# Optimization experiments

Measured on AMD Instinct MI355X. Metric: run time of the kernel, lower is better.

## Reference

```python
import math
import jax, jax.numpy as jnp
import numpy as np

B, T, D = 128, 243, 1024   # batch, motion frames, latent_dim
N, L = 77, 512             # text tokens, text_latent_dim
H = 16                     # num_head -> head_dim 64
EPS = 1e-5


def _ln(x, g, b):
    m = x.mean(-1, keepdims=True)
    v = jnp.var(x, axis=-1, keepdims=True)
    return (x - m) * jax.lax.rsqrt(v + EPS) * g + b


def setup_inputs() -> dict:
    key = jax.random.key(0)
    ks = jax.random.split(key, 16)
    s = 0.02
    return {
        "x": jax.random.normal(ks[0], (B, T, D), jnp.float32),
        "xf": jax.random.normal(ks[1], (B, N, L), jnp.float32),
        "emb": jax.random.normal(ks[2], (B, T, D), jnp.float32),
        "ln_g": jnp.ones((D,), jnp.float32), "ln_b": jnp.zeros((D,), jnp.float32),
        "tln_g": jnp.ones((L,), jnp.float32), "tln_b": jnp.zeros((L,), jnp.float32),
        "Wq": jax.random.normal(ks[3], (D, D), jnp.float32) * s,
        "bq": jnp.zeros((D,), jnp.float32),
        "Wk": jax.random.normal(ks[4], (L, D), jnp.float32) * s,
        "bk": jnp.zeros((D,), jnp.float32),
        "Wv": jax.random.normal(ks[5], (L, D), jnp.float32) * s,
        "bv": jnp.zeros((D,), jnp.float32),
        "We": jax.random.normal(ks[6], (D, 2 * D), jnp.float32) * s,  # emb_layers Linear(time_embed_dim=D, 2D)
        "be": jnp.zeros((2 * D,), jnp.float32),
        "ln2_g": jnp.ones((D,), jnp.float32), "ln2_b": jnp.zeros((D,), jnp.float32),
        "Wo": jax.random.normal(ks[7], (D, D), jnp.float32) * s,     # zero_module in torch; random here for non-trivial baseline
        "bo": jnp.zeros((D,), jnp.float32),
    }


def reference(x, xf, emb, ln_g, ln_b, tln_g, tln_b, Wq, bq, Wk, bk, Wv, bv,
              We, be, ln2_g, ln2_b, Wo, bo):
    B_, T_, D_ = x.shape
    dh = D_ // H
    # cross-attention: queries from motion tokens, keys/values from text
    q = (_ln(x, ln_g, ln_b) @ Wq + bq).reshape(B_, T_, H, dh)
    xfn = _ln(xf, tln_g, tln_b)
    k = (xfn @ Wk + bk).reshape(B_, -1, H, dh)
    v = (xfn @ Wv + bv).reshape(B_, -1, H, dh)
    att = jnp.einsum('bthd,bnhd->btnh', q, k) / math.sqrt(dh)  # (B,T,N,H)
    w = jax.nn.softmax(att, axis=2)                            # softmax over text tokens; dropout is eval-mode identity
    y = jnp.einsum('btnh,bnhd->bthd', w, v).reshape(B_, T_, D_)
    # StylizationBlock (AdaLN): emb viewed (B,T,D), only first timestep used
    emb_out = (jax.nn.silu(emb) @ We + be)[:, 0:1, :]          # (B,1,2D)
    scale, shift = jnp.split(emb_out, 2, axis=2)
    h = _ln(y, ln2_g, ln2_b) * (1.0 + scale) + shift
    h = jax.nn.silu(h) @ Wo + bo
    return x + h
```

## Files before the change

kernel.cpp:

```cpp
#include <hip/hip_runtime.h>
#include <cstdint>

typedef __attribute__((ext_vector_type(8))) __bf16 bf16x8;
typedef __attribute__((ext_vector_type(4))) float f32x4;
typedef __attribute__((ext_vector_type(8))) unsigned short ushort8v;

__device__ __forceinline__ float b2f(unsigned short u) {
    union { uint32_t i; float f; } w; w.i = ((uint32_t)u) << 16; return w.f;
}
__device__ __forceinline__ unsigned short f2b(float f) {
    union { uint32_t i; float f; } w; w.f = f;
    uint32_t r = (w.i + 0x7FFFu + ((w.i >> 16) & 1u)) >> 16;
    return (unsigned short)r;
}

__device__ __forceinline__ void gl16(const unsigned short* g, unsigned short* l) {
    __builtin_amdgcn_global_load_lds(
        (const __attribute__((address_space(1))) void*)g,
        (__attribute__((address_space(3))) void*)l,
        16, 0, 0);
}

__global__ __launch_bounds__(256) void k_cvt_all(
    const float* __restrict__ Wq, const float* __restrict__ Wk,
    const float* __restrict__ Wv, const float* __restrict__ We,
    const float* __restrict__ Wo,
    unsigned short* __restrict__ wqt, unsigned short* __restrict__ wkvt,
    unsigned short* __restrict__ wet, unsigned short* __restrict__ wot) {
    __shared__ float s[32][33];
    int bid = blockIdx.x;
    const float* in; unsigned short* out; int R, C;
    if (bid < 1024)      { in = Wq; out = wqt;              R = 1024; C = 1024; }
    else if (bid < 1536) { bid -= 1024; in = Wk; out = wkvt;             R = 512;  C = 1024; }
    else if (bid < 2048) { bid -= 1536; in = Wv; out = wkvt + 1024 * 512; R = 512;  C = 1024; }
    else if (bid < 4096) { bid -= 2048; in = We; out = wet;              R = 1024; C = 2048; }
    else                 { bid -= 4096; in = Wo; out = wot;              R = 1024; C = 1024; }
    const int ctiles = C >> 5;
    const int c0 = (bid % ctiles) * 32, r0 = (bid / ctiles) * 32;
    const int tx = threadIdx.x & 31, ty = threadIdx.x >> 5;
#pragma unroll
    for (int i = 0; i < 4; ++i)
        s[ty + i * 8][tx] = in[(size_t)(r0 + ty + i * 8) * C + c0 + tx];
    __syncthreads();
#pragma unroll
    for (int i = 0; i < 4; ++i)
        out[(size_t)(c0 + ty + i * 8) * R + r0 + tx] = f2b(s[tx][ty + i * 8]);
}

template <int DIM>
__global__ __launch_bounds__(256) void k_ln(const float* __restrict__ in,
                                            const float* __restrict__ g,
                                            const float* __restrict__ b,
                                            unsigned short* __restrict__ out) {
    const int row = blockIdx.x * 4 + (threadIdx.x >> 6);
    const int ln = threadIdx.x & 63;
    constexpr int PL = DIM / 64;
    float v[PL];
    const size_t base = (size_t)row * DIM + (size_t)ln * PL;
    const float4* p4 = (const float4*)(in + base);
#pragma unroll
    for (int c = 0; c < PL / 4; ++c) {
        const float4 t = p4[c];
        v[c * 4 + 0] = t.x; v[c * 4 + 1] = t.y; v[c * 4 + 2] = t.z; v[c * 4 + 3] = t.w;
    }
    float s = 0.f, s2 = 0.f;
#pragma unroll
    for (int c = 0; c < PL; ++c) { s += v[c]; s2 += v[c] * v[c]; }
    for (int o = 1; o < 64; o <<= 1) { s += __shfl_xor(s, o); s2 += __shfl_xor(s2, o); }
    const float mean = s / DIM;
    const float rstd = rsqrtf(s2 / DIM - mean * mean + 1e-5f);
    const float4* g4 = (const float4*)(g + ln * PL);
    const float4* b4 = (const float4*)(b + ln * PL);
#pragma unroll
    for (int c0 = 0; c0 < PL; c0 += 8) {
        ushort8v yv;
#pragma unroll
        for (int j = 0; j < 8; ++j) {
            const int c = c0 + j;
            const float gg = ((const float*)g4)[c];
            const float bb = ((const float*)b4)[c];
            yv[j] = f2b((v[c] - mean) * rstd * gg + bb);
        }
        *(ushort8v*)(out + base + c0) = yv;
    }
}

__global__ __launch_bounds__(256) void k_silu(const float* __restrict__ emb,
                                              unsigned short* __restrict__ se) {
    const int i = blockIdx.x * 256 + threadIdx.x;
    const int b = i >> 10, k = i & 1023;
    const float f = emb[(size_t)b * (243 * 1024) + k];
    se[i] = f2b(f / (1.f + __expf(-f)));
}

template <int EPI>
__global__ __launch_bounds__(512, 2) void k_mm(
    const unsigned short* __restrict__ A, const unsigned short* __restrict__ Bt,
    const float* __restrict__ bias0, const float* __restrict__ bias1,
    unsigned short* __restrict__ C0, unsigned short* __restrict__ C1,
    float* __restrict__ Cf, const float* __restrict__ X,
    int N, int K) {
    __shared__ __align__(16) unsigned short sA[128 * 64];
    __shared__ __align__(16) unsigned short sB[256 * 64];
    const int tid = threadIdx.x, wv = tid >> 6, ln = tid & 63;
    const int wm = wv >> 2, wn = wv & 3;
    const int ln15 = ln & 15, lg = ln >> 4;

    const int NN = N >> 8;
    const int nwg = gridDim.x;
    const int wg = blockIdx.x;
    const int q = nwg >> 3, r = nwg & 7;
    const int xcd = wg & 7, idx = wg >> 3;
    const int u = (xcd < r) ? (xcd * (q + 1) + idx)
                            : (r * (q + 1) + (xcd - r) * q + idx);
    const int m0 = (u / NN) * 128, n0 = (u % NN) * 256;

    const f32x4 fz = {0.f, 0.f, 0.f, 0.f};
    f32x4 acc[4][4];
#pragma unroll
    for (int i = 0; i < 4; ++i)
#pragma unroll
        for (int j = 0; j < 4; ++j) acc[i][j] = fz;

    const int lrow = ln >> 3;
    const int sslot = (ln & 7) ^ lrow;
    const unsigned short* ga = A + (size_t)(m0 + wv * 16 + lrow) * K + sslot * 8;
    const unsigned short* gb = Bt + (size_t)(n0 + wv * 32 + lrow) * K + sslot * 8;
    unsigned short* const lA = sA + (wv * 16) * 64;
    unsigned short* const lB = sB + (wv * 32) * 64;

    for (int k0 = 0; k0 < K; k0 += 64) {
#pragma unroll
        for (int i = 0; i < 2; ++i)
            gl16(ga + k0 + (size_t)i * 8 * K, lA + i * 8 * 64);
#pragma unroll
        for (int i = 0; i < 4; ++i)
            gl16(gb + k0 + (size_t)i * 8 * K, lB + i * 8 * 64);
        __syncthreads();
        bf16x8 af[4][2], bf[4][2];
#pragma unroll
        for (int i = 0; i < 4; ++i) {
            const int ra2 = wm * 64 + i * 16 + ln15;
            const int rb2 = wn * 64 + i * 16 + ln15;
#pragma unroll
            for (int ks = 0; ks < 2; ++ks) {
                const int slot = ks * 4 + lg;
                af[i][ks] = *(const bf16x8*)(sA + ra2 * 64 + ((slot ^ (ra2 & 7)) * 8));
                bf[i][ks] = *(const bf16x8*)(sB + rb2 * 64 + ((slot ^ (rb2 & 7)) * 8));
            }
        }
#pragma unroll
        for (int mi = 0; mi < 4; ++mi)
#pragma unroll
            for (int ni = 0; ni < 4; ++ni) {
                acc[mi][ni] = __builtin_amdgcn_mfma_f32_16x16x32_bf16(af[mi][0], bf[ni][0], acc[mi][ni], 0, 0, 0);
                acc[mi][ni] = __builtin_amdgcn_mfma_f32_16x16x32_bf16(af[mi][1], bf[ni][1], acc[mi][ni], 0, 0, 0);
            }
        __syncthreads();
    }

    const int colB = n0 + wn * 64;
    const int rowB = m0 + wm * 64;
#pragma unroll
    for (int mi = 0; mi < 4; ++mi) {
#pragma unroll
        for (int ni = 0; ni < 4; ++ni) {
            const int col = colB + ni * 16 + ln15;
            const int row = rowB + mi * 16 + lg * 4;
            float bvv;
            if (EPI == 2) bvv = (col < 1024) ? bias0[col] : bias1[col - 1024];
            else bvv = bias0[col];
#pragma unroll
            for (int r2 = 0; r2 < 4; ++r2) {
                const float v = acc[mi][ni][r2] + bvv;
                if (EPI == 0) {
                    C0[(size_t)(row + r2) * N + col] = f2b(v);
                } else if (EPI == 1) {
                    Cf[(size_t)(row + r2) * N + col] = v + X[(size_t)(row + r2) * N + col];
                } else if (EPI == 2) {
                    if (col < 1024) C0[(size_t)(row + r2) * 1024 + col] = f2b(v);
                    else C1[(size_t)(row + r2) * 1024 + (col - 1024)] = f2b(v);
                } else {
                    Cf[(size_t)(row + r2) * N + col] = v;
                }
            }
        }
    }
}

__global__ __launch_bounds__(256, 2) void k_attn_m(const unsigned short* __restrict__ Q,
                                                   const unsigned short* __restrict__ Kb,
                                                   const unsigned short* __restrict__ Vb,
                                                   unsigned short* __restrict__ Y) {
    __shared__ __align__(16) unsigned short sK[80 * 64];
    __shared__ __align__(16) unsigned short sV[64 * 96];
    __shared__ __align__(16) unsigned short sP[4][16 * 104];
    const int bh = blockIdx.x;
    const int b = bh >> 4, h = bh & 15;
    const int tid = threadIdx.x, wv = tid >> 6, ln = tid & 63;
    const int ln15 = ln & 15, lg = ln >> 4;

    for (int c = tid; c < 640; c += 256) {
        const int n = c >> 3, ci = c & 7;
        uint4 val = make_uint4(0u, 0u, 0u, 0u);
        if (n < 77) val = *(const uint4*)(Kb + (size_t)(b * 77 + n) * 1024 + h * 64 + ci * 8);
        *(uint4*)((char*)sK + n * 128 + ((ci * 16) ^ ((n & 7) << 4))) = val;
    }
    for (int i = tid; i < 64 * 96; i += 256) {
        const int d = i / 96, n = i - d * 96;
        unsigned short val = 0;
        if (n < 77) val = Vb[(size_t)(b * 77 + n) * 1024 + h * 64 + d];
        sV[i] = val;
    }
    for (int i = ln; i < 16 * 24; i += 64) {
        const int rr = i / 24, cc = i - rr * 24;
        sP[wv][rr * 104 + 80 + cc] = 0;
    }
    bf16x8 qf[4][2];
    const size_t qbase = (size_t)b * (243 * 1024) + h * 64;
#pragma unroll
    for (int mi = 0; mi < 4; ++mi) {
        int t = wv * 64 + mi * 16 + ln15;
        if (t > 242) t = 242;
#pragma unroll
        for (int ks = 0; ks < 2; ++ks)
            qf[mi][ks] = *(const bf16x8*)(Q + qbase + (size_t)t * 1024 + ks * 32 + lg * 8);
    }
    __syncthreads();

    const f32x4 fz = {0.f, 0.f, 0.f, 0.f};
    f32x4 yacc[4][4];
#pragma unroll
    for (int i = 0; i < 4; ++i)
#pragma unroll
        for (int j = 0; j < 4; ++j) yacc[i][j] = fz;

#pragma unroll
    for (int mi = 0; mi < 4; ++mi) {
        f32x4 sc[5];
#pragma unroll
        for (int ci = 0; ci < 5; ++ci) sc[ci] = fz;
#pragma unroll
        for (int ci = 0; ci < 5; ++ci) {
            const int n = ci * 16 + ln15;
#pragma unroll
            for (int ks = 0; ks < 2; ++ks) {
                const int kk = ks * 32 + lg * 8;
                bf16x8 kf = *(const bf16x8*)((const char*)sK + n * 128 + ((kk * 2) ^ ((n & 7) << 4)));
                sc[ci] = __builtin_amdgcn_mfma_f32_16x16x32_bf16(qf[mi][ks], kf, sc[ci], 0, 0, 0);
            }
        }
#pragma unroll
        for (int r = 0; r < 4; ++r) {
            float e[5];
            float mx = -1e30f;
#pragma unroll
            for (int ci = 0; ci < 5; ++ci) {
                const int n = ci * 16 + ln15;
                const float vv = (n < 77) ? sc[ci][r] * 0.125f : -1e30f;
                e[ci] = vv;
                mx = fmaxf(mx, vv);
            }
            mx = fmaxf(mx, __shfl_xor(mx, 1));
            mx = fmaxf(mx, __shfl_xor(mx, 2));
            mx = fmaxf(mx, __shfl_xor(mx, 4));
            mx = fmaxf(mx, __shfl_xor(mx, 8));
            float ssum = 0.f;
#pragma unroll
            for (int ci = 0; ci < 5; ++ci) {
                const int n = ci * 16 + ln15;
                const float ev = (n < 77) ? __expf(e[ci] - mx) : 0.f;
                e[ci] = ev;
                ssum += ev;
            }
            ssum += __shfl_xor(ssum, 1);
            ssum += __shfl_xor(ssum, 2);
            ssum += __shfl_xor(ssum, 4);
            ssum += __shfl_xor(ssum, 8);
            const float inv = 1.f / ssum;
            const int prow = lg * 4 + r;
#pragma unroll
            for (int ci = 0; ci < 5; ++ci)
                sP[wv][prow * 104 + ci * 16 + ln15] = f2b(e[ci] * inv);
        }
#pragma unroll
        for (int ks = 0; ks < 3; ++ks) {
            bf16x8 pa = *(const bf16x8*)(sP[wv] + ln15 * 104 + ks * 32 + lg * 8);
#pragma unroll
            for (int di = 0; di < 4; ++di) {
                bf16x8 vf = *(const bf16x8*)(sV + (di * 16 + ln15) * 96 + ks * 32 + lg * 8);
                yacc[mi][di] = __builtin_amdgcn_mfma_f32_16x16x32_bf16(pa, vf, yacc[mi][di], 0, 0, 0);
            }
        }
    }
    const size_t ybase = (size_t)b * (243 * 1024) + h * 64;
#pragma unroll
    for (int mi = 0; mi < 4; ++mi)
#pragma unroll
        for (int di = 0; di < 4; ++di)
#pragma unroll
            for (int r = 0; r < 4; ++r) {
                const int t = wv * 64 + mi * 16 + lg * 4 + r;
                if (t < 243) Y[ybase + (size_t)t * 1024 + di * 16 + ln15] = f2b(yacc[mi][di][r]);
            }
}

__global__ __launch_bounds__(256) void k_act(const unsigned short* __restrict__ y,
                                             const float* __restrict__ eo,
                                             const float* __restrict__ g,
                                             const float* __restrict__ b,
                                             unsigned short* __restrict__ out) {
    const int row = blockIdx.x * 4 + (threadIdx.x >> 6);
    const int ln = threadIdx.x & 63;
    const int bb = row / 243;
    float v[16];
    const size_t base = (size_t)row * 1024 + ln * 16;
#pragma unroll
    for (int c0 = 0; c0 < 16; c0 += 8) {
        const ushort8v t = *(const ushort8v*)(y + base + c0);
#pragma unroll
        for (int j = 0; j < 8; ++j) v[c0 + j] = b2f(t[j]);
    }
    float s = 0.f, s2 = 0.f;
#pragma unroll
    for (int c = 0; c < 16; ++c) { s += v[c]; s2 += v[c] * v[c]; }
    for (int o = 1; o < 64; o <<= 1) { s += __shfl_xor(s, o); s2 += __shfl_xor(s2, o); }
    const float mean = s / 1024.f;
    const float rstd = rsqrtf(s2 / 1024.f - mean * mean + 1e-5f);
    const float* gp = g + ln * 16;
    const float* bp = b + ln * 16;
    const float* sc = eo + (size_t)bb * 2048 + ln * 16;
    const float* sh = sc + 1024;
#pragma unroll
    for (int c0 = 0; c0 < 16; c0 += 8) {
        ushort8v yv;
#pragma unroll
        for (int j = 0; j < 8; ++j) {
            const int c = c0 + j;
            const float nl = (v[c] - mean) * rstd * gp[c] + bp[c];
            const float hh = nl * (1.f + sc[c]) + sh[c];
            yv[j] = f2b(hh / (1.f + __expf(-hh)));
        }
        *(ushort8v*)(out + base + c0) = yv;
    }
}

extern "C" void kernel_launch(void* const* d_in, const int* in_sizes, int n_in,
                              void* d_out, int out_size, void* d_ws, size_t ws_size,
                              hipStream_t stream) {
    (void)in_sizes; (void)n_in; (void)out_size; (void)ws_size;

    const float* x     = (const float*)d_in[0];
    const float* xf    = (const float*)d_in[1];
    const float* emb   = (const float*)d_in[2];
    const float* ln_g  = (const float*)d_in[3];
    const float* ln_b  = (const float*)d_in[4];
    const float* tln_g = (const float*)d_in[5];
    const float* tln_b = (const float*)d_in[6];
    const float* Wq    = (const float*)d_in[7];
    const float* bq    = (const float*)d_in[8];
    const float* Wk    = (const float*)d_in[9];
    const float* bk    = (const float*)d_in[10];
    const float* Wv    = (const float*)d_in[11];
    const float* bv    = (const float*)d_in[12];
    const float* We    = (const float*)d_in[13];
    const float* be    = (const float*)d_in[14];
    const float* ln2_g = (const float*)d_in[15];
    const float* ln2_b = (const float*)d_in[16];
    const float* Wo    = (const float*)d_in[17];
    const float* bo    = (const float*)d_in[18];
    float* outp = (float*)d_out;

    char* ws = (char*)d_ws;
    constexpr size_t o_wq   = 0;
    constexpr size_t o_wkv  = o_wq + 2097152;
    constexpr size_t o_we   = o_wkv + 2097152;
    constexpr size_t o_wo   = o_we + 4194304;
    constexpr size_t o_se   = o_wo + 2097152;
    constexpr size_t o_eo   = o_se + 262144;
    constexpr size_t o_xn   = o_eo + 1048576;
    constexpr size_t o_qb   = o_xn + 63700992;
    constexpr size_t o_xfn  = o_qb + 63700992;
    constexpr size_t o_kb   = o_xfn + 10092544;
    constexpr size_t o_vb   = o_kb + 20185088;

    unsigned short* wqt  = (unsigned short*)(ws + o_wq);
    unsigned short* wkvt = (unsigned short*)(ws + o_wkv);
    unsigned short* wet  = (unsigned short*)(ws + o_we);
    unsigned short* wot  = (unsigned short*)(ws + o_wo);
    unsigned short* se   = (unsigned short*)(ws + o_se);
    float*          eo   = (float*)(ws + o_eo);
    unsigned short* xn   = (unsigned short*)(ws + o_xn);
    unsigned short* yb   = xn;
    unsigned short* qb   = (unsigned short*)(ws + o_qb);
    unsigned short* actb = qb;
    unsigned short* xfn  = (unsigned short*)(ws + o_xfn);
    unsigned short* kb   = (unsigned short*)(ws + o_kb);
    unsigned short* vb   = (unsigned short*)(ws + o_vb);

    k_ln<1024><<<7776, 256, 0, stream>>>(x, ln_g, ln_b, xn);
    k_ln<512><<<2464, 256, 0, stream>>>(xf, tln_g, tln_b, xfn);
    k_silu<<<512, 256, 0, stream>>>(emb, se);
    k_cvt_all<<<5120, 256, 0, stream>>>(Wq, Wk, Wv, We, Wo, wqt, wkvt, wet, wot);

    k_mm<3><<<8, 512, 0, stream>>>(se, wet, be, nullptr,
                                   nullptr, nullptr, eo, nullptr, 2048, 1024);

    k_mm<0><<<243 * 4, 512, 0, stream>>>(xn, wqt, bq, nullptr,
                                         qb, nullptr, nullptr, nullptr, 1024, 1024);
    k_mm<2><<<77 * 8, 512, 0, stream>>>(xfn, wkvt, bk, bv,
                                        kb, vb, nullptr, nullptr, 2048, 512);

    k_attn_m<<<2048, 256, 0, stream>>>(qb, kb, vb, yb);

    k_act<<<7776, 256, 0, stream>>>(yb, eo, ln2_g, ln2_b, actb);

    k_mm<1><<<243 * 4, 512, 0, stream>>>(actb, wot, bo, nullptr,
                                         nullptr, nullptr, outp, x, 1024, 1024);
}
```

Before: 393.7 us.

## Merge Q, KV and emb GEMMs into one launch and coalesce attention I/O

After: 353.5 us. 1.11x faster.

```diff
diff --git a/kernel.cpp b/kernel.cpp
--- a/kernel.cpp
+++ b/kernel.cpp
@@ -19,6 +19,13 @@
         (const __attribute__((address_space(1))) void*)g,
         (__attribute__((address_space(3))) void*)l,
         16, 0, 0);
+}
+
+__device__ __forceinline__ int swz8(int wg, int nwg) {
+    const int q = nwg >> 3, r = nwg & 7;
+    const int xcd = wg & 7, idx = wg >> 3;
+    return (xcd < r) ? (xcd * (q + 1) + idx)
+                     : (r * (q + 1) + (xcd - r) * q + idx);
 }
 
 __global__ __launch_bounds__(256) void k_cvt_all(
@@ -93,26 +100,17 @@
     se[i] = f2b(f / (1.f + __expf(-f)));
 }
 
-template <int EPI>
-__global__ __launch_bounds__(512, 2) void k_mm(
+__device__ __forceinline__ void mm_body(
+    int u, int NN,
     const unsigned short* __restrict__ A, const unsigned short* __restrict__ Bt,
     const float* __restrict__ bias0, const float* __restrict__ bias1,
     unsigned short* __restrict__ C0, unsigned short* __restrict__ C1,
     float* __restrict__ Cf, const float* __restrict__ X,
-    int N, int K) {
-    __shared__ __align__(16) unsigned short sA[128 * 64];
-    __shared__ __align__(16) unsigned short sB[256 * 64];
+    int N, int K, int epi,
+    unsigned short* sA, unsigned short* sB) {
     const int tid = threadIdx.x, wv = tid >> 6, ln = tid & 63;
     const int wm = wv >> 2, wn = wv & 3;
     const int ln15 = ln & 15, lg = ln >> 4;
-
-    const int NN = N >> 8;
-    const int nwg = gridDim.x;
-    const int wg = blockIdx.x;
-    const int q = nwg >> 3, r = nwg & 7;
-    const int xcd = wg & 7, idx = wg >> 3;
-    const int u = (xcd < r) ? (xcd * (q + 1) + idx)
-                            : (r * (q + 1) + (xcd - r) * q + idx);
     const int m0 = (u / NN) * 128, n0 = (u % NN) * 256;
 
     const f32x4 fz = {0.f, 0.f, 0.f, 0.f};
@@ -168,16 +166,16 @@
             const int col = colB + ni * 16 + ln15;
             const int row = rowB + mi * 16 + lg * 4;
             float bvv;
-            if (EPI == 2) bvv = (col < 1024) ? bias0[col] : bias1[col - 1024];
+            if (epi == 2) bvv = (col < 1024) ? bias0[col] : bias1[col - 1024];
             else bvv = bias0[col];
 #pragma unroll
             for (int r2 = 0; r2 < 4; ++r2) {
                 const float v = acc[mi][ni][r2] + bvv;
-                if (EPI == 0) {
+                if (epi == 0) {
                     C0[(size_t)(row + r2) * N + col] = f2b(v);
-                } else if (EPI == 1) {
+                } else if (epi == 1) {
                     Cf[(size_t)(row + r2) * N + col] = v + X[(size_t)(row + r2) * N + col];
-                } else if (EPI == 2) {
+                } else if (epi == 2) {
                     if (col < 1024) C0[(size_t)(row + r2) * 1024 + col] = f2b(v);
                     else C1[(size_t)(row + r2) * 1024 + (col - 1024)] = f2b(v);
                 } else {
@@ -188,11 +186,45 @@
     }
 }
 
+__global__ __launch_bounds__(512, 2) void k_mm3(
+    const unsigned short* __restrict__ xn, const unsigned short* __restrict__ wqt,
+    const float* __restrict__ bq, unsigned short* __restrict__ qb,
+    const unsigned short* __restrict__ xfn, const unsigned short* __restrict__ wkvt,
+    const float* __restrict__ bk, const float* __restrict__ bv,
+    unsigned short* __restrict__ kb, unsigned short* __restrict__ vb,
+    const unsigned short* __restrict__ se, const unsigned short* __restrict__ wet,
+    const float* __restrict__ be, float* __restrict__ eo) {
+    __shared__ __align__(16) unsigned short sA[128 * 64];
+    __shared__ __align__(16) unsigned short sB[256 * 64];
+    const int wg = blockIdx.x;
+    if (wg < 972) {
+        mm_body(swz8(wg, 972), 4, xn, wqt, bq, nullptr, qb, nullptr, nullptr, nullptr,
+                1024, 1024, 0, sA, sB);
+    } else if (wg < 1588) {
+        mm_body(swz8(wg - 972, 616), 8, xfn, wkvt, bk, bv, kb, vb, nullptr, nullptr,
+                2048, 512, 2, sA, sB);
+    } else {
+        mm_body(wg - 1588, 8, se, wet, be, nullptr, nullptr, nullptr, eo, nullptr,
+                2048, 1024, 3, sA, sB);
+    }
+}
+
+__global__ __launch_bounds__(512, 2) void k_mm1(
+    const unsigned short* __restrict__ actb, const unsigned short* __restrict__ wot,
+    const float* __restrict__ bo, const float* __restrict__ x,
+    float* __restrict__ outp) {
+    __shared__ __align__(16) unsigned short sA[128 * 64];
+    __shared__ __align__(16) unsigned short sB[256 * 64];
+    mm_body(swz8(blockIdx.x, 972), 4, actb, wot, bo, nullptr, nullptr, nullptr,
+            outp, x, 1024, 1024, 1, sA, sB);
+}
+
 __global__ __launch_bounds__(256, 2) void k_attn_m(const unsigned short* __restrict__ Q,
                                                    const unsigned short* __restrict__ Kb,
                                                    const unsigned short* __restrict__ Vb,
                                                    unsigned short* __restrict__ Y) {
     __shared__ __align__(16) unsigned short sK[80 * 64];
+    __shared__ __align__(16) unsigned short sVr[80 * 72];
     __shared__ __align__(16) unsigned short sV[64 * 96];
     __shared__ __align__(16) unsigned short sP[4][16 * 104];
     const int bh = blockIdx.x;
@@ -202,39 +234,38 @@
 
     for (int c = tid; c < 640; c += 256) {
         const int n = c >> 3, ci = c & 7;
-        uint4 val = make_uint4(0u, 0u, 0u, 0u);
-        if (n < 77) val = *(const uint4*)(Kb + (size_t)(b * 77 + n) * 1024 + h * 64 + ci * 8);
-        *(uint4*)((char*)sK + n * 128 + ((ci * 16) ^ ((n & 7) << 4))) = val;
-    }
+        uint4 kv = make_uint4(0u, 0u, 0u, 0u), vv = make_uint4(0u, 0u, 0u, 0u);
+        if (n < 77) {
+            const size_t o = (size_t)(b * 77 + n) * 1024 + h * 64 + ci * 8;
+            kv = *(const uint4*)(Kb + o);
+            vv = *(const uint4*)(Vb + o);
+        }
+        *(uint4*)((char*)sK + n * 128 + ((ci * 16) ^ ((n & 7) << 4))) = kv;
+        *(uint4*)(sVr + n * 72 + ci * 8) = vv;
+    }
+    bf16x8 qf[4][2];
+    const size_t qbase = (size_t)b * (243 * 1024) + h * 64;
+#pragma unroll
+    for (int mi = 0; mi < 4; ++mi) {
+        int t = wv * 64 + mi * 16 + ln15;
+        if (t > 242) t = 242;
+#pragma unroll
+        for (int ks = 0; ks < 2; ++ks)
+            qf[mi][ks] = *(const bf16x8*)(Q + qbase + (size_t)t * 1024 + ks * 32 + lg * 8);
+    }
+    __syncthreads();
+
     for (int i = tid; i < 64 * 96; i += 256) {
         const int d = i / 96, n = i - d * 96;
-        unsigned short val = 0;
-        if (n < 77) val = Vb[(size_t)(b * 77 + n) * 1024 + h * 64 + d];
-        sV[i] = val;
+        sV[i] = (n < 80) ? sVr[n * 72 + d] : (unsigned short)0;
     }
     for (int i = ln; i < 16 * 24; i += 64) {
         const int rr = i / 24, cc = i - rr * 24;
         sP[wv][rr * 104 + 80 + cc] = 0;
     }
-    bf16x8 qf[4][2];
-    const size_t qbase = (size_t)b * (243 * 1024) + h * 64;
-#pragma unroll
-    for (int mi = 0; mi < 4; ++mi) {
-        int t = wv * 64 + mi * 16 + ln15;
-        if (t > 242) t = 242;
-#pragma unroll
-        for (int ks = 0; ks < 2; ++ks)
-            qf[mi][ks] = *(const bf16x8*)(Q + qbase + (size_t)t * 1024 + ks * 32 + lg * 8);
-    }
     __syncthreads();
 
     const f32x4 fz = {0.f, 0.f, 0.f, 0.f};
-    f32x4 yacc[4][4];
-#pragma unroll
-    for (int i = 0; i < 4; ++i)
-#pragma unroll
-        for (int j = 0; j < 4; ++j) yacc[i][j] = fz;
-
 #pragma unroll
     for (int mi = 0; mi < 4; ++mi) {
         f32x4 sc[5];
@@ -283,26 +314,34 @@
             for (int ci = 0; ci < 5; ++ci)
                 sP[wv][prow * 104 + ci * 16 + ln15] = f2b(e[ci] * inv);
         }
+        f32x4 ya[4];
+#pragma unroll
+        for (int di = 0; di < 4; ++di) ya[di] = fz;
 #pragma unroll
         for (int ks = 0; ks < 3; ++ks) {
             bf16x8 pa = *(const bf16x8*)(sP[wv] + ln15 * 104 + ks * 32 + lg * 8);
 #pragma unroll
             for (int di = 0; di < 4; ++di) {
                 bf16x8 vf = *(const bf16x8*)(sV + (di * 16 + ln15) * 96 + ks * 32 + lg * 8);
-                yacc[mi][di] = __builtin_amdgcn_mfma_f32_16x16x32_bf16(pa, vf, yacc[mi][di], 0, 0, 0);
-            }
-        }
-    }
-    const size_t ybase = (size_t)b * (243 * 1024) + h * 64;
-#pragma unroll
-    for (int mi = 0; mi < 4; ++mi)
+                ya[di] = __builtin_amdgcn_mfma_f32_16x16x32_bf16(pa, vf, ya[di], 0, 0, 0);
+            }
+        }
+        unsigned short* sy = sP[wv];
 #pragma unroll
         for (int di = 0; di < 4; ++di)
 #pragma unroll
-            for (int r = 0; r < 4; ++r) {
-                const int t = wv * 64 + mi * 16 + lg * 4 + r;
-                if (t < 243) Y[ybase + (size_t)t * 1024 + di * 16 + ln15] = f2b(yacc[mi][di][r]);
-            }
+            for (int r = 0; r < 4; ++r)
+                sy[(lg * 4 + r) * 72 + di * 16 + ln15] = f2b(ya[di][r]);
+        const int tb = wv * 64 + mi * 16;
+#pragma unroll
+        for (int j = 0; j < 2; ++j) {
+            const int k = ln * 2 + j;
+            const int row = k >> 3, off = (k & 7) * 8;
+            const int t = tb + row;
+            if (t < 243)
+                *(uint4*)(Y + qbase + (size_t)t * 1024 + off) = *(const uint4*)(sy + row * 72 + off);
+        }
+    }
 }
 
 __global__ __launch_bounds__(256) void k_act(const unsigned short* __restrict__ y,
@@ -403,18 +442,13 @@
     k_silu<<<512, 256, 0, stream>>>(emb, se);
     k_cvt_all<<<5120, 256, 0, stream>>>(Wq, Wk, Wv, We, Wo, wqt, wkvt, wet, wot);
 
-    k_mm<3><<<8, 512, 0, stream>>>(se, wet, be, nullptr,
-                                   nullptr, nullptr, eo, nullptr, 2048, 1024);
-
-    k_mm<0><<<243 * 4, 512, 0, stream>>>(xn, wqt, bq, nullptr,
-                                         qb, nullptr, nullptr, nullptr, 1024, 1024);
-    k_mm<2><<<77 * 8, 512, 0, stream>>>(xfn, wkvt, bk, bv,
-                                        kb, vb, nullptr, nullptr, 2048, 512);
+    k_mm3<<<1596, 512, 0, stream>>>(xn, wqt, bq, qb,
+                                    xfn, wkvt, bk, bv, kb, vb,
+                                    se, wet, be, eo);
 
     k_attn_m<<<2048, 256, 0, stream>>>(qb, kb, vb, yb);
 
     k_act<<<7776, 256, 0, stream>>>(yb, eo, ln2_g, ln2_b, actb);
 
-    k_mm<1><<<243 * 4, 512, 0, stream>>>(actb, wot, bo, nullptr,
-                                         nullptr, nullptr, outp, x, 1024, 1024);
-}
+    k_mm1<<<972, 512, 0, stream>>>(actb, wot, bo, x, outp);
+}
```
